# Kernel optimization log

Hardware: AMD Instinct MI355X
Metric: run time of the kernel (lower is better)

The kernel has to match this reference:

```python
import jax, jax.numpy as jnp
import numpy as np

B, T, IN, H, N, M = 64, 64, 256, 512, 4096, 128
EPS = 1e-8


def setup_inputs() -> dict:
    key = jax.random.key(0)
    ks = jax.random.split(key, 24)
    s = 0.05
    w = lambda k, shape: jax.random.normal(k, shape, jnp.float32) * s
    return {
        "x": jax.random.normal(ks[0], (B, T, 1, IN), jnp.float32),
        "mem0": jax.random.uniform(ks[1], (B, N, M), jnp.float32) * 0.1,
        "Wx": w(ks[2], (IN, H)),
        "Wr": w(ks[3], (M, H)),
        "bC": jnp.zeros((H,), jnp.float32),
        "r_Wk": w(ks[4], (H, M)), "r_bk": jnp.zeros((M,), jnp.float32),
        "r_Wbeta": w(ks[5], (H, 1)), "r_Wg": w(ks[6], (H, 1)),
        "r_Ws": w(ks[7], (H, 3)), "r_Wgam": w(ks[8], (H, 1)),
        "w_Wk": w(ks[9], (H, M)), "w_bk": jnp.zeros((M,), jnp.float32),
        "w_Wbeta": w(ks[10], (H, 1)), "w_Wg": w(ks[11], (H, 1)),
        "w_Ws": w(ks[12], (H, 3)), "w_Wgam": w(ks[13], (H, 1)),
        "w_We": w(ks[14], (H, M)), "w_Wa": w(ks[15], (H, M)),
    }


def _address(h, w_prev, mem, Wk, bk, Wbeta, Wg, Ws, Wgam):
    # h: [B,H], w_prev: [B,N], mem: [B,N,M]
    k = jnp.tanh(h @ Wk + bk)                      # [B,M]
    beta = jax.nn.softplus(h @ Wbeta)              # [B,1]
    g = jax.nn.sigmoid(h @ Wg)                     # [B,1]
    s = jax.nn.softmax(h @ Ws, axis=-1)            # [B,3]
    gamma = 1.0 + jax.nn.softplus(h @ Wgam)        # [B,1]
    # cosine similarity content addressing
    dot = jnp.einsum('bnm,bm->bn', mem, k)         # [B,N]
    mnorm = jnp.linalg.norm(mem, axis=-1)          # [B,N]
    knorm = jnp.linalg.norm(k, axis=-1, keepdims=True)  # [B,1]
    wc = jax.nn.softmax(beta * dot / (mnorm * knorm + EPS), axis=-1)
    wg = g * wc + (1.0 - g) * w_prev               # [B,N]
    # circular shift with 3 taps {-1, 0, +1}
    wt = (s[:, 0:1] * jnp.roll(wg, -1, axis=1)
          + s[:, 1:2] * wg
          + s[:, 2:3] * jnp.roll(wg, 1, axis=1))
    wp = (wt + EPS) ** gamma                        # sharpen
    return wp / jnp.sum(wp, axis=-1, keepdims=True)


def reference(x, mem0, Wx, Wr, bC,
              r_Wk, r_bk, r_Wbeta, r_Wg, r_Ws, r_Wgam,
              w_Wk, w_bk, w_Wbeta, w_Wg, w_Ws, w_Wgam, w_We, w_Wa):
    xt = x.reshape(B, T, -1).transpose(1, 0, 2)    # [T,B,IN]
    w0 = jnp.zeros((B, N), jnp.float32).at[0, 0].set(1.0)
    h0 = jnp.zeros((B, H), jnp.float32)

    def step(carry, x_t):
        mem, wr, ww, h = carry
        # write to memory using previous hidden and ww (erase then add)
        e = jax.nn.sigmoid(h @ w_We)               # [B,M]
        a = jnp.tanh(h @ w_Wa)                     # [B,M]
        mem = mem * (1.0 - ww[:, :, None] * e[:, None, :]) \
              + ww[:, :, None] * a[:, None, :]     # [B,N,M]
        # read
        r = jnp.einsum('bn,bnm->bm', wr, mem)      # [B,M]
        # controller step
        h = jnp.tanh(x_t @ Wx + r @ Wr + bC)       # [B,H]
        # new addressing weights
        wr = _address(h, wr, mem, r_Wk, r_bk, r_Wbeta, r_Wg, r_Ws, r_Wgam)
        ww = _address(h, ww, mem, w_Wk, w_bk, w_Wbeta, w_Wg, w_Ws, w_Wgam)
        return (mem, wr, ww, h), None

    (mem, wr, ww, h), _ = jax.lax.scan(step, (mem0, w0, w0, h0), xt)
    return h                                       # last hidden state [B,H]
```

## Files before the change

### kernel.cpp

```cpp
#include <hip/hip_runtime.h>
#include <hip/hip_bf16.h>
#include <math.h>

#define BB 64
#define TT 64
#define INDIM 256
#define HH 512
#define NN 4096
#define MM 128
#define SS 32
#define ROWS 128
#define WC 544
#define EPSF 1e-8f

__device__ __forceinline__ float fsig(float x){ return 1.f/(1.f+__expf(-x)); }
__device__ __forceinline__ float ftanh(float x){ return 1.f - 2.f/(__expf(2.f*x)+1.f); }
__device__ __forceinline__ float softplusf_(float x){ return (x>20.f)? x : log1pf(expf(x)); }

__device__ __forceinline__ void unpack2(unsigned u, float& lo, float& hi){
  lo = __uint_as_float(u << 16);
  hi = __uint_as_float(u & 0xffff0000u);
}
__device__ __forceinline__ unsigned packrn(float a, float b){
  __hip_bfloat162 p = __float22bfloat162_rn(make_float2(a,b));
  return *reinterpret_cast<unsigned*>(&p);
}

__global__ __launch_bounds__(256) void kCvt(const float* __restrict__ src,
                                            uint4* __restrict__ dst){
  const size_t i = (size_t)blockIdx.x*blockDim.x + threadIdx.x;
  const float4 f0 = *(const float4*)(src + i*8);
  const float4 f1 = *(const float4*)(src + i*8 + 4);
  uint4 q;
  q.x = packrn(f0.x, f0.y); q.y = packrn(f0.z, f0.w);
  q.z = packrn(f1.x, f1.y); q.w = packrn(f1.z, f1.w);
  dst[i] = q;
}

__global__ void kInit(float* wr, float* ww, float* headout){
  const int i = blockIdx.x*blockDim.x + threadIdx.x;
  if (i < BB*NN){ const float v = (i==0)? 1.f : 0.f; wr[i]=v; ww[i]=v; }
  if (i < BB*WC) headout[i]=0.f;
}

__global__ __launch_bounds__(576) void kPack(
    const float* __restrict__ rWk, const float* __restrict__ wWk,
    const float* __restrict__ wWe, const float* __restrict__ wWa,
    const float* __restrict__ rWbeta, const float* __restrict__ rWg,
    const float* __restrict__ rWs, const float* __restrict__ rWgam,
    const float* __restrict__ wWbeta, const float* __restrict__ wWg,
    const float* __restrict__ wWs, const float* __restrict__ wWgam,
    float* __restrict__ Wall)
{
  const int j = blockIdx.x, c = threadIdx.x;
  if (c >= WC) return;
  float v = 0.f;
  if      (c < 128) v = rWk[(size_t)j*128 + c];
  else if (c < 256) v = wWk[(size_t)j*128 + c-128];
  else if (c < 384) v = wWe[(size_t)j*128 + c-256];
  else if (c < 512) v = wWa[(size_t)j*128 + c-384];
  else {
    const int cc = c - 512;
    switch (cc){
      case 0:  v = rWbeta[j]; break;
      case 1:  v = rWg[j];    break;
      case 2: case 3: case 4: v = rWs[(size_t)j*3 + cc-2]; break;
      case 5:  v = rWgam[j];  break;
      case 6:  v = wWbeta[j]; break;
      case 7:  v = wWg[j];    break;
      case 8: case 9: case 10: v = wWs[(size_t)j*3 + cc-8]; break;
      case 11: v = wWgam[j];  break;
      default: v = 0.f; break;
    }
  }
  Wall[(size_t)j*WC + c] = v;
}

__global__ __launch_bounds__(512) void kPre(const float* __restrict__ x,
                                            const float* __restrict__ Wx,
                                            const float* __restrict__ bC,
                                            float* __restrict__ xwx){
  const int bt0 = blockIdx.x*16, t = threadIdx.x;
  __shared__ float xs[INDIM][16];
  for (int lin = t; lin < 16*INDIM; lin += 512){
    const int ii = lin & 255, r = lin >> 8;
    xs[ii][r] = x[(size_t)(bt0+r)*INDIM + ii];
  }
  __syncthreads();
  float accv[16];
  #pragma unroll
  for (int r=0;r<16;++r) accv[r]=0.f;
  for (int ii=0; ii<INDIM; ++ii){
    const float w = Wx[(size_t)ii*HH + t];
    const float4* xp = (const float4*)&xs[ii][0];
    const float4 x0=xp[0], x1=xp[1], x2=xp[2], x3=xp[3];
    accv[0]+=x0.x*w; accv[1]+=x0.y*w; accv[2]+=x0.z*w; accv[3]+=x0.w*w;
    accv[4]+=x1.x*w; accv[5]+=x1.y*w; accv[6]+=x1.z*w; accv[7]+=x1.w*w;
    accv[8]+=x2.x*w; accv[9]+=x2.y*w; accv[10]+=x2.z*w; accv[11]+=x2.w*w;
    accv[12]+=x3.x*w; accv[13]+=x3.y*w; accv[14]+=x3.z*w; accv[15]+=x3.w*w;
  }
  const float bc = bC[t];
  #pragma unroll
  for (int r=0;r<16;++r)
    xwx[(size_t)(bt0+r)*HH + t] = accv[r] + bc;
}

__global__ __launch_bounds__(256) void kA(
    const float* __restrict__ headout,
    const float* __restrict__ wrG, const float* __restrict__ wwG,
    uint4* __restrict__ mem, float* __restrict__ rpart, float* __restrict__ mnormG)
{
  const int b = blockIdx.y;
  const int n0 = blockIdx.x * ROWS;
  const int t = threadIdx.x;
  const int grp = t >> 4, lane = t & 15;
  const int m0 = lane * 8;
  const float* HO = headout + (size_t)b*WC;
  float ev[8], av[8];
  #pragma unroll
  for (int j=0;j<8;++j){
    ev[j] = fsig (HO[256 + m0 + j]);
    av[j] = ftanh(HO[384 + m0 + j]);
  }
  float wwv[8], wrv[8];
  #pragma unroll
  for (int rr=0; rr<8; ++rr){
    const int n = n0 + rr*16 + grp;
    wwv[rr] = wwG[b*NN+n];
    wrv[rr] = wrG[b*NN+n];
  }
  float racc[8];
  #pragma unroll
  for (int j=0;j<8;++j) racc[j]=0.f;
  __shared__ float lr[16][128];
  const size_t base4 = ((size_t)b*NN + n0)*(MM/8) + (size_t)grp*(MM/8) + lane;
  uint4 q = mem[base4];
  #pragma unroll
  for (int rr=0; rr<8; ++rr){
    uint4 qn;
    if (rr<7) qn = mem[base4 + (size_t)(rr+1)*16*(MM/8)];
    const int n = n0 + rr*16 + grp;
    float v[8];
    unpack2(q.x, v[0], v[1]); unpack2(q.y, v[2], v[3]);
    unpack2(q.z, v[4], v[5]); unpack2(q.w, v[6], v[7]);
    float sq = 0.f;
    const float w = wwv[rr], wr_ = wrv[rr];
    #pragma unroll
    for (int j=0;j<8;++j){
      v[j] = v[j]*(1.f - w*ev[j]) + w*av[j];
      racc[j] += wr_*v[j];
      sq += v[j]*v[j];
    }
    uint4 q2;
    q2.x = packrn(v[0],v[1]); q2.y = packrn(v[2],v[3]);
    q2.z = packrn(v[4],v[5]); q2.w = packrn(v[6],v[7]);
    mem[base4 + (size_t)rr*16*(MM/8)] = q2;
    #pragma unroll
    for (int msk=1; msk<16; msk<<=1) sq += __shfl_xor(sq, msk);
    if (lane==0) mnormG[b*NN+n] = sqrtf(sq);
    q = qn;
  }
  #pragma unroll
  for (int j=0;j<8;++j) lr[grp][m0+j] = racc[j];
  __syncthreads();
  if (t < MM){
    float s=0.f;
    #pragma unroll
    for (int g=0; g<16; ++g) s += lr[g][t];
    rpart[((size_t)b*SS + blockIdx.x)*MM + t] = s;
  }
}

__global__ __launch_bounds__(256) void kH(
    const float* __restrict__ xwx, int tstep,
    const float* __restrict__ Wr, const float* __restrict__ rpart,
    float* __restrict__ hG, float* __restrict__ outG)
{
  const int c0 = blockIdx.x*32, b0 = blockIdx.y*8;
  const int tid = threadIdx.x;
  const int bb = tid>>5, cc = tid&31;
  __shared__ float rsS[8][128];
  __shared__ float WrS[128][32];
  for (int lin = tid; lin < 8*128; lin += 256){
    const int rb = lin>>7, m = lin&127;
    float s = 0.f;
    #pragma unroll
    for (int ss=0; ss<SS; ++ss)
      s += rpart[((size_t)(b0+rb)*SS + ss)*MM + m];
    rsS[rb][m] = s;
  }
  for (int lin = tid; lin < 128*32; lin += 256){
    const int m = lin>>5, c = lin&31;
    WrS[m][c] = Wr[(size_t)m*HH + c0 + c];
  }
  __syncthreads();
  float acc = xwx[((size_t)(b0+bb)*TT + tstep)*HH + c0 + cc];
  #pragma unroll 8
  for (int m=0;m<128;++m) acc += rsS[bb][m]*WrS[m][cc];
  const float hv = ftanh(acc);
  hG[(size_t)(b0+bb)*HH + c0 + cc] = hv;
  if (tstep == TT-1) outG[(size_t)(b0+bb)*HH + c0 + cc] = hv;
}

__global__ __launch_bounds__(256) void kB2(
    const float* __restrict__ hG, const float* __restrict__ Wall,
    float* __restrict__ headout)
{
  const int c0 = blockIdx.x*32, b0 = blockIdx.y*8;
  const int tid = threadIdx.x;
  const int bb = tid>>5, cc = tid&31;
  __shared__ float hs[8][HH];
  __shared__ float WsS[64][32];
  for (int lin = tid; lin < 8*HH; lin += 256)
    hs[lin>>9][lin&511] = hG[(size_t)(b0+(lin>>9))*HH + (lin&511)];
  float acc = 0.f;
  for (int ks=0; ks<8; ++ks){
    __syncthreads();
    for (int lin = tid; lin < 64*32; lin += 256){
      const int m = lin>>5, c = lin&31;
      WsS[m][c] = Wall[(size_t)(ks*64+m)*WC + c0 + c];
    }
    __syncthreads();
    #pragma unroll 8
    for (int m=0;m<64;++m) acc += hs[bb][ks*64+m]*WsS[m][cc];
  }
  headout[(size_t)(b0+bb)*WC + c0 + cc] = acc;
}

__global__ __launch_bounds__(256) void kC(
    const uint4* __restrict__ mem, const float* __restrict__ headout,
    const float* __restrict__ rbk, const float* __restrict__ wbk,
    float* __restrict__ dotrG, float* __restrict__ dotwG)
{
  const int b = blockIdx.y;
  const int n0 = blockIdx.x * ROWS;
  const int t = threadIdx.x, grp=t>>4, lane=t&15;
  const int m0 = lane*8;
  const float* HO = headout + (size_t)b*WC;
  float krv[8], kwv[8];
  #pragma unroll
  for (int j=0;j<8;++j){
    krv[j] = ftanh(HO[m0+j]     + rbk[m0+j]);
    kwv[j] = ftanh(HO[128+m0+j] + wbk[m0+j]);
  }
  const size_t base4 = ((size_t)b*NN + n0)*(MM/8) + (size_t)grp*(MM/8) + lane;
  uint4 q = mem[base4];
  #pragma unroll
  for (int rr=0; rr<8; ++rr){
    uint4 qn;
    if (rr<7) qn = mem[base4 + (size_t)(rr+1)*16*(MM/8)];
    const int n = n0 + rr*16 + grp;
    float v[8];
    unpack2(q.x, v[0], v[1]); unpack2(q.y, v[2], v[3]);
    unpack2(q.z, v[4], v[5]); unpack2(q.w, v[6], v[7]);
    float dr=0.f, dw=0.f;
    #pragma unroll
    for (int j=0;j<8;++j){ dr += v[j]*krv[j]; dw += v[j]*kwv[j]; }
    #pragma unroll
    for (int msk=1; msk<16; msk<<=1){
      dr += __shfl_xor(dr, msk);
      dw += __shfl_xor(dw, msk);
    }
    if (lane==0){ dotrG[b*NN+n]=dr; dotwG[b*NN+n]=dw; }
    q = qn;
  }
}

__device__ __forceinline__ float blockSum256(float v, volatile float* sc){
  #pragma unroll
  for (int m=1;m<64;m<<=1) v += __shfl_xor(v,m);
  __syncthreads();
  if ((threadIdx.x&63)==0) sc[threadIdx.x>>6]=v;
  __syncthreads();
  return sc[0]+sc[1]+sc[2]+sc[3];
}

__global__ __launch_bounds__(256) void kD(
    const float* __restrict__ dotrG, const float* __restrict__ dotwG,
    const float* __restrict__ mnormG, const float* __restrict__ headout,
    const float* __restrict__ rbk, const float* __restrict__ wbk,
    float* __restrict__ wrG, float* __restrict__ wwG)
{
  const int b = blockIdx.x, head = blockIdx.y, t = threadIdx.x;
  __shared__ float wg[NN];
  __shared__ float sc[4];
  __shared__ float sb[8];
  __shared__ float kred[2];
  const float* HO = headout + (size_t)b*WC;
  const float* bk = head? wbk : rbk;
  if (t < 128){
    const float km = ftanh(HO[head*128 + t] + bk[t]);
    float s = km*km;
    #pragma unroll
    for (int m=1;m<64;m<<=1) s += __shfl_xor(s, m);
    if ((t&63)==0) kred[t>>6]=s;
  }
  __syncthreads();
  if (t==0){
    const int sbase = 512 + head*6;
    sb[0] = softplusf_(HO[sbase+0]);
    sb[1] = fsig(HO[sbase+1]);
    sb[2] = 1.f + softplusf_(HO[sbase+5]);
    const float s0=HO[sbase+2], s1=HO[sbase+3], s2=HO[sbase+4];
    const float mx = fmaxf(s0, fmaxf(s1,s2));
    const float e0=__expf(s0-mx), e1=__expf(s1-mx), e2=__expf(s2-mx);
    const float inv3=1.f/(e0+e1+e2);
    sb[3]=e0*inv3; sb[4]=e1*inv3; sb[5]=e2*inv3;
    sb[6] = sqrtf(kred[0]+kred[1]);
  }
  __syncthreads();
  const float* dot = head? dotwG : dotrG;
  float* wv = head? wwG : wrG;
  const float beta=sb[0], g=sb[1], gamma=sb[2];
  const float s0=sb[3], s1=sb[4], s2=sb[5], knorm=sb[6];
  float sim[16]; float sum=0.f;
  #pragma unroll
  for (int i=0;i<16;++i){
    const int n = i*256 + t;
    const float d  = dot[(size_t)b*NN+n];
    const float mn = mnormG[(size_t)b*NN+n];
    sim[i] = __expf(beta*d/(mn*knorm + EPSF));
    sum += sim[i];
  }
  sum = blockSum256(sum, sc);
  const float inv = 1.f/sum;
  #pragma unroll
  for (int i=0;i<16;++i){
    const int n = i*256 + t;
    wg[n] = g*sim[i]*inv + (1.f-g)*wv[(size_t)b*NN+n];
  }
  __syncthreads();
  float wp[16]; float ps=0.f;
  #pragma unroll
  for (int i=0;i<16;++i){
    const int n = i*256 + t;
    const float wt = s0*wg[(n+1)&(NN-1)] + s1*wg[n] + s2*wg[(n-1)&(NN-1)];
    wp[i] = __powf(wt + EPSF, gamma);
    ps += wp[i];
  }
  ps = blockSum256(ps, sc);
  const float ip = 1.f/ps;
  #pragma unroll
  for (int i=0;i<16;++i){
    const int n = i*256 + t;
    wv[(size_t)b*NN+n] = wp[i]*ip;
  }
}

extern "C" void kernel_launch(void* const* d_in, const int* in_sizes, int n_in,
                              void* d_out, int out_size, void* d_ws, size_t ws_size,
                              hipStream_t stream)
{
  const float* x     = (const float*)d_in[0];
  const float* mem0  = (const float*)d_in[1];
  const float* Wx    = (const float*)d_in[2];
  const float* Wr    = (const float*)d_in[3];
  const float* bC    = (const float*)d_in[4];
  const float* rWk   = (const float*)d_in[5];
  const float* rbk   = (const float*)d_in[6];
  const float* rWbeta= (const float*)d_in[7];
  const float* rWg   = (const float*)d_in[8];
  const float* rWs   = (const float*)d_in[9];
  const float* rWgam = (const float*)d_in[10];
  const float* wWk   = (const float*)d_in[11];
  const float* wbk   = (const float*)d_in[12];
  const float* wWbeta= (const float*)d_in[13];
  const float* wWg   = (const float*)d_in[14];
  const float* wWs   = (const float*)d_in[15];
  const float* wWgam = (const float*)d_in[16];
  const float* wWe   = (const float*)d_in[17];
  const float* wWa   = (const float*)d_in[18];

  float* ws = (float*)d_ws;
  size_t o = 0;
  uint4* mem    = (uint4*)(ws + o); o += (size_t)BB*NN*MM/2;
  float* wr     = ws + o; o += (size_t)BB*NN;
  float* ww     = ws + o; o += (size_t)BB*NN;
  float* rpart  = ws + o; o += (size_t)BB*SS*MM;
  float* mnorm  = ws + o; o += (size_t)BB*NN;
  float* dotr   = ws + o; o += (size_t)BB*NN;
  float* dotw   = ws + o; o += (size_t)BB*NN;
  float* xwx    = ws + o; o += (size_t)BB*TT*HH;
  float* hG     = ws + o; o += (size_t)BB*HH;
  float* headout= ws + o; o += (size_t)BB*WC;
  float* Wall   = ws + o; o += (size_t)HH*WC;

  kCvt<<<(BB*NN*MM/8)/256, 256, 0, stream>>>(mem0, mem);
  kInit<<<(BB*NN+255)/256, 256, 0, stream>>>(wr, ww, headout);
  kPack<<<HH, 576, 0, stream>>>(rWk, wWk, wWe, wWa,
                                rWbeta, rWg, rWs, rWgam,
                                wWbeta, wWg, wWs, wWgam, Wall);
  kPre<<<(BB*TT)/16, 512, 0, stream>>>(x, Wx, bC, xwx);

  for (int t=0; t<TT; ++t){
    kA<<<dim3(SS,BB), 256, 0, stream>>>(headout, wr, ww, mem, rpart, mnorm);
    kH<<<dim3(16,8), 256, 0, stream>>>(xwx, t, Wr, rpart, hG, (float*)d_out);
    if (t < TT-1){
      kB2<<<dim3(17,8), 256, 0, stream>>>(hG, Wall, headout);
      kC<<<dim3(SS,BB), 256, 0, stream>>>(mem, headout, rbk, wbk, dotr, dotw);
      kD<<<dim3(BB,2), 256, 0, stream>>>(dotr, dotw, mnorm, headout,
                                         rbk, wbk, wr, ww);
    }
  }
}
```

Baseline: 4.759 ms.

## Fuse controller hidden update and head projection into one per-batch kernel

Merges the kH (hidden state) and kB2 (head projection) kernels into a single kernel kHB with one 1024-thread block per batch row. The hidden vector stays in shared memory instead of going through a global buffer, and one launch per timestep is removed. In exchange each block now reads the full Wr and Wall matrices from global memory without shared-memory tiling. Only 64 blocks run, which may leave most of the GPU idle and make these reads slower per step.

```diff
diff --git a/kernel.cpp b/kernel.cpp
--- a/kernel.cpp
+++ b/kernel.cpp
@@ -171,60 +171,66 @@
   }
 }
 
-__global__ __launch_bounds__(256) void kH(
+__global__ __launch_bounds__(1024) void kHB(
     const float* __restrict__ xwx, int tstep,
-    const float* __restrict__ Wr, const float* __restrict__ rpart,
-    float* __restrict__ hG, float* __restrict__ outG)
-{
-  const int c0 = blockIdx.x*32, b0 = blockIdx.y*8;
-  const int tid = threadIdx.x;
-  const int bb = tid>>5, cc = tid&31;
-  __shared__ float rsS[8][128];
-  __shared__ float WrS[128][32];
-  for (int lin = tid; lin < 8*128; lin += 256){
-    const int rb = lin>>7, m = lin&127;
-    float s = 0.f;
-    #pragma unroll
-    for (int ss=0; ss<SS; ++ss)
-      s += rpart[((size_t)(b0+rb)*SS + ss)*MM + m];
-    rsS[rb][m] = s;
-  }
-  for (int lin = tid; lin < 128*32; lin += 256){
-    const int m = lin>>5, c = lin&31;
-    WrS[m][c] = Wr[(size_t)m*HH + c0 + c];
-  }
-  __syncthreads();
-  float acc = xwx[((size_t)(b0+bb)*TT + tstep)*HH + c0 + cc];
-  #pragma unroll 8
-  for (int m=0;m<128;++m) acc += rsS[bb][m]*WrS[m][cc];
-  const float hv = ftanh(acc);
-  hG[(size_t)(b0+bb)*HH + c0 + cc] = hv;
-  if (tstep == TT-1) outG[(size_t)(b0+bb)*HH + c0 + cc] = hv;
-}
-
-__global__ __launch_bounds__(256) void kB2(
-    const float* __restrict__ hG, const float* __restrict__ Wall,
-    float* __restrict__ headout)
-{
-  const int c0 = blockIdx.x*32, b0 = blockIdx.y*8;
-  const int tid = threadIdx.x;
-  const int bb = tid>>5, cc = tid&31;
-  __shared__ float hs[8][HH];
-  __shared__ float WsS[64][32];
-  for (int lin = tid; lin < 8*HH; lin += 256)
-    hs[lin>>9][lin&511] = hG[(size_t)(b0+(lin>>9))*HH + (lin&511)];
-  float acc = 0.f;
-  for (int ks=0; ks<8; ++ks){
-    __syncthreads();
-    for (int lin = tid; lin < 64*32; lin += 256){
-      const int m = lin>>5, c = lin&31;
-      WsS[m][c] = Wall[(size_t)(ks*64+m)*WC + c0 + c];
+    const float* __restrict__ Wr, const float* __restrict__ Wall,
+    const float* __restrict__ rpart,
+    float* __restrict__ headout, float* __restrict__ outG)
+{
+  const int b = blockIdx.x, t = threadIdx.x;
+  __shared__ float rs[MM], hs[HH], lrH[8][MM], hd[8][MM];
+  {
+    const int part = t>>7, m = t&127;
+    float s=0.f;
+    #pragma unroll
+    for (int i=0;i<4;++i)
+      s += rpart[((size_t)b*SS + part + i*8)*MM + m];
+    lrH[part][m] = s;
+  }
+  __syncthreads();
+  if (t < MM){
+    float s=0.f;
+    #pragma unroll
+    for (int p=0;p<8;++p) s += lrH[p][t];
+    rs[t]=s;
+  }
+  __syncthreads();
+  if (t < HH){
+    float acc = xwx[((size_t)b*TT + tstep)*HH + t];
+    #pragma unroll 4
+    for (int m=0;m<MM;++m) acc += rs[m]*Wr[(size_t)m*HH + t];
+    const float hv = ftanh(acc);
+    hs[t]=hv;
+    if (tstep == TT-1) outG[(size_t)b*HH+t]=hv;
+  }
+  __syncthreads();
+  if (tstep == TT-1) return;
+  {
+    const int q = t >> 7, m = t & 127;
+    const int head = q & 3, jh = q >> 2;
+    const int col = head*128 + m;
+    float acc = 0.f;
+    const int j0 = jh*256;
+    #pragma unroll 4
+    for (int j=j0; j<j0+256; ++j) acc += hs[j]*Wall[(size_t)j*WC + col];
+    hd[q][m] = acc;
+  }
+  {
+    const int wv = t>>6, ln = t&63;
+    if (wv < 12){
+      const int c = 512 + wv;
+      float acc=0.f;
+      for (int j=ln; j<HH; j+=64) acc += hs[j]*Wall[(size_t)j*WC + c];
+      #pragma unroll
+      for (int msk=1; msk<64; msk<<=1) acc += __shfl_xor(acc, msk);
+      if (ln==0) headout[(size_t)b*WC + c] = acc;
     }
-    __syncthreads();
-    #pragma unroll 8
-    for (int m=0;m<64;++m) acc += hs[bb][ks*64+m]*WsS[m][cc];
-  }
-  headout[(size_t)(b0+bb)*WC + c0 + cc] = acc;
+  }
+  __syncthreads();
+  if (t < 512){
+    const int q2 = t>>7, m = t&127;
+    headout[(size_t)b*WC + q2*128 + m] = hd[q2][m] + hd[q2+4][m];
+  }
 }
 
 __global__ __launch_bounds__(256) void kC(
@@ -381,7 +387,6 @@
   float* dotr   = ws + o; o += (size_t)BB*NN;
   float* dotw   = ws + o; o += (size_t)BB*NN;
   float* xwx    = ws + o; o += (size_t)BB*TT*HH;
-  float* hG     = ws + o; o += (size_t)BB*HH;
   float* headout= ws + o; o += (size_t)BB*WC;
   float* Wall   = ws + o; o += (size_t)HH*WC;
 
@@ -394,9 +399,9 @@
 
   for (int t=0; t<TT; ++t){
     kA<<<dim3(SS,BB), 256, 0, stream>>>(headout, wr, ww, mem, rpart, mnorm);
-    kH<<<dim3(16,8), 256, 0, stream>>>(xwx, t, Wr, rpart, hG, (float*)d_out);
+    kHB<<<BB, 1024, 0, stream>>>(xwx, t, Wr, Wall, rpart,
+                                 headout, (float*)d_out);
     if (t < TT-1){
-      kB2<<<dim3(17,8), 256, 0, stream>>>(hG, Wall, headout);
       kC<<<dim3(SS,BB), 256, 0, stream>>>(mem, headout, rbk, wbk, dotr, dotw);
       kD<<<dim3(BB,2), 256, 0, stream>>>(dotr, dotw, mnorm, headout,
                                          rbk, wbk, wr, ww);
```

Result: slower. 5.221 ms (+9.7%).
